# Performance work log

Measured on AMD Instinct MI355X. Metric: run time of the kernel, lower is better.

## Reference

```python
import jax, jax.numpy as jnp
import numpy as np

# --- config (matches init_kwargs) ---
D_MODEL = 512
N_HEADS = 8
DIM_HEAD = D_MODEL // N_HEADS  # 64
BUCKET_SIZE = 64
N_HASHES = 4
B = 4
N = 4096
SELF_ATTN_VALUE = -5e4  # TOKEN_SELF_ATTN_VALUE in reformer_pytorch


def setup_inputs() -> dict:
    key = jax.random.key(0)
    ks = jax.random.split(key, 8)
    n_buckets = N // BUCKET_SIZE
    dh = N_HEADS * DIM_HEAD
    return {
        "queries": jax.random.normal(ks[0], (B, N, D_MODEL), jnp.float32),
        "keys": jax.random.normal(ks[1], (B, N, D_MODEL), jnp.float32),      # unused by module
        "values": jax.random.normal(ks[2], (B, N, D_MODEL), jnp.float32),    # unused by module
        "W_qk": jax.random.normal(ks[3], (D_MODEL, dh), jnp.float32) / np.float32(np.sqrt(D_MODEL)),
        "W_v": jax.random.normal(ks[4], (D_MODEL, dh), jnp.float32) / np.float32(np.sqrt(D_MODEL)),
        "W_out": jax.random.normal(ks[5], (dh, D_MODEL), jnp.float32) / np.float32(np.sqrt(dh)),
        "b_out": jnp.zeros((D_MODEL,), jnp.float32),
        # random LSH rotations: generated fresh (non-learnable) in torch; fixed here for determinism
        "rotations": jax.random.normal(ks[6], (DIM_HEAD, N_HASHES, n_buckets // 2), jnp.float32),
    }


def _look_one_back(x):
    # concat each chunk with the previous chunk along the within-chunk axis
    return jnp.concatenate([x, jnp.roll(x, 1, axis=1)], axis=2)


def lsh_attention(qk, v, rotations):
    # qk, v: (BH, T, dh) shared-QK LSH attention (reformer_pytorch LSHAttention)
    bh, T, dh = qk.shape
    n_buckets = T // BUCKET_SIZE
    total = N_HASHES * T

    # --- hash_vectors: random rotations + argmax over [R, -R] ---
    rotated = jnp.einsum('btf,fhi->bhti', qk, rotations)          # (bh, n_hashes, T, nb/2)
    rotated = jnp.concatenate([rotated, -rotated], axis=-1)       # (bh, n_hashes, T, nb)
    buckets = jnp.argmax(rotated, axis=-1)                        # (bh, n_hashes, T)
    offsets = (jnp.arange(N_HASHES) * n_buckets)[None, :, None]
    buckets = (buckets + offsets).reshape(bh, total)

    # --- stable sort by (bucket, position); keys are unique ---
    ticker = jnp.broadcast_to(jnp.arange(total)[None, :], (bh, total))
    buckets_and_t = T * buckets + (ticker % T)
    sticker = jnp.argsort(buckets_and_t, axis=-1)                 # (bh, total)
    undo_sort = jnp.argsort(sticker, axis=-1)
    st = sticker % T                                              # original positions, sorted

    sqk = jnp.take_along_axis(qk, st[:, :, None], axis=1)         # (bh, total, dh)
    sv = jnp.take_along_axis(v, st[:, :, None], axis=1)

    # --- chunk into bins; attend within chunk + one chunk back ---
    chunks = N_HASHES * n_buckets                                 # per-chunk len == BUCKET_SIZE
    bq_t = st.reshape(bh, chunks, -1)
    bqk = sqk.reshape(bh, chunks, -1, dh)
    bv = sv.reshape(bh, chunks, -1, dh)

    bq = bqk
    bk = bqk / jnp.maximum(jnp.linalg.norm(bqk, axis=-1, keepdims=True), 1e-12)  # F.normalize

    bk = _look_one_back(bk)       # (bh, chunks, 2*bs, dh)
    bv = _look_one_back(bv)
    bkv_t = _look_one_back(bq_t)  # (bh, chunks, 2*bs)

    dots = jnp.einsum('bcie,bcje->bcij', bq, bk) * (dh ** -0.5)   # (bh, chunks, bs, 2*bs)
    self_mask = bq_t[:, :, :, None] == bkv_t[:, :, None, :]
    dots = jnp.where(self_mask, SELF_ATTN_VALUE, dots)

    lse = jax.scipy.special.logsumexp(dots, axis=-1, keepdims=True)
    probs = jnp.exp(dots - lse)
    bo = jnp.einsum('bcij,bcje->bcie', probs, bv)                 # (bh, chunks, bs, dh)

    so = bo.reshape(bh, total, dh)
    slogits = lse.reshape(bh, total)
    o = jnp.take_along_axis(so, undo_sort[:, :, None], axis=1)
    logits = jnp.take_along_axis(slogits, undo_sort, axis=1)

    o = o.reshape(bh, N_HASHES, T, dh)
    logits = logits.reshape(bh, N_HASHES, T, 1)
    # combine hash rounds by softmax over per-round logsumexps
    w = jnp.exp(logits - jax.scipy.special.logsumexp(logits, axis=1, keepdims=True))
    return jnp.sum(o * w, axis=1)                                 # (bh, T, dh)


def reference(queries, keys, values, W_qk, W_v, W_out, b_out, rotations):
    Bsz, T, _ = queries.shape
    qk = queries @ W_qk                                           # (B, T, H*dh), no bias
    v = queries @ W_v

    def merge(x):
        return x.reshape(Bsz, T, N_HEADS, DIM_HEAD).transpose(0, 2, 1, 3).reshape(Bsz * N_HEADS, T, DIM_HEAD)

    out = lsh_attention(merge(qk), merge(v), rotations)           # (B*H, T, dh)
    out = out.reshape(Bsz, N_HEADS, T, DIM_HEAD).transpose(0, 2, 1, 3).reshape(Bsz, T, N_HEADS * DIM_HEAD)
    return out @ W_out + b_out                                    # to_out (with bias)
```

## Files before the change

### kernel.cpp

```cpp
#include <hip/hip_runtime.h>

typedef unsigned int uint32;
typedef _Float16 f16;
typedef _Float16 f16x8 __attribute__((ext_vector_type(8)));
typedef float f32x4 __attribute__((ext_vector_type(4)));
typedef unsigned short u16x8 __attribute__((ext_vector_type(8)));

#define B_SZ 4
#define T_SZ 4096
#define DMODEL 512
#define NHEAD 8
#define DH 64
#define NHASH 4
#define BH (B_SZ*NHEAD)
#define NBUCK 256
#define TOT (NHASH*T_SZ)
#define M_TOK (B_SZ*T_SZ)

#define KSTRIDE 72
#define PSTRIDE 136

#define AMB_TAU 1.5e-3f

__global__ __launch_bounds__(256) void kprep(
    const float* __restrict__ Wqk, const float* __restrict__ Wv,
    const float* __restrict__ Wout, f16* __restrict__ Wth, f16* __restrict__ Wtl,
    const float* __restrict__ rot, f16* __restrict__ rotTh, f16* __restrict__ rotTl,
    const float* __restrict__ qin, f16* __restrict__ Ah, f16* __restrict__ Al,
    int* __restrict__ amb_cnt)
{
  int bx = blockIdx.x;
  if (bx == 0 && threadIdx.x == 0) *amb_cnt = 0;
  if (bx < 3072){
    int gid = bx*256 + threadIdx.x;
    int n = gid >> 9, k = gid & 511;
    int sel = n >> 9, col = n & 511;
    const float* src = (sel==0)? Wqk : (sel==1)? Wv : Wout;
    float v = src[(size_t)k*512 + col];
    f16 h = (f16)v;
    Wth[gid] = h;
    Wtl[gid] = (f16)(v - (float)h);
  } else if (bx < 3104){
    int gid = (bx - 3072)*256 + threadIdx.x;
    int n = gid >> 6, dd = gid & 63;
    float v = rot[dd*128 + n];
    f16 h = (f16)v;
    rotTh[gid] = h;
    rotTl[gid] = (f16)(v - (float)h);
  } else {
    size_t gid = (size_t)(bx - 3104)*256 + threadIdx.x;
    const float4* src = (const float4*)(qin) + gid*2;
    float4 x0 = src[0], x1 = src[1];
    float v[8] = {x0.x,x0.y,x0.z,x0.w, x1.x,x1.y,x1.z,x1.w};
    f16x8 h, l;
    #pragma unroll
    for (int e=0;e<8;e++){ f16 hh=(f16)v[e]; h[e]=hh; l[e]=(f16)(v[e]-(float)hh); }
    ((f16x8*)Ah)[gid] = h;
    ((f16x8*)Al)[gid] = l;
  }
}

__global__ __launch_bounds__(256) void g_qkv(const f16* __restrict__ Ah,
    const f16* __restrict__ Al, const f16* __restrict__ Wth, const f16* __restrict__ Wtl,
    f16* __restrict__ qk16, f16* __restrict__ qkl, f16* __restrict__ v16)
{
  __shared__ f16 ah[128*KSTRIDE], al[128*KSTRIDE], bh[128*KSTRIDE], bl[128*KSTRIDE];
  int tid = threadIdx.x;
  int m0 = blockIdx.x*128, n0 = blockIdx.y*128;
  int w = tid >> 6, lane = tid & 63;
  int wm = w >> 1, wn = w & 1;
  int c_lane = lane & 15, quad = lane >> 4;

  f32x4 acc[4][4];
  #pragma unroll
  for (int mi=0;mi<4;mi++)
    #pragma unroll
    for (int ni=0;ni<4;ni++) acc[mi][ni] = (f32x4){0.f,0.f,0.f,0.f};

  int sr = tid >> 1, sc = (tid & 1) * 32;
  for (int kc=0; kc<8; kc++){
    int k0 = kc*64;
    {
      const f16x8* pah = (const f16x8*)(Ah + (size_t)(m0+sr)*512 + k0 + sc);
      const f16x8* pal = (const f16x8*)(Al + (size_t)(m0+sr)*512 + k0 + sc);
      const f16x8* pbh = (const f16x8*)(Wth + (size_t)(n0+sr)*512 + k0 + sc);
      const f16x8* pbl = (const f16x8*)(Wtl + (size_t)(n0+sr)*512 + k0 + sc);
      f16x8* dah = (f16x8*)&ah[sr*KSTRIDE + sc];
      f16x8* dal = (f16x8*)&al[sr*KSTRIDE + sc];
      f16x8* dbh = (f16x8*)&bh[sr*KSTRIDE + sc];
      f16x8* dbl = (f16x8*)&bl[sr*KSTRIDE + sc];
      #pragma unroll
      for (int i=0;i<4;i++){ dah[i]=pah[i]; dal[i]=pal[i]; dbh[i]=pbh[i]; dbl[i]=pbl[i]; }
    }
    __syncthreads();
    f16x8 fah[4][2], fal[4][2], fbh[4][2], fbl[4][2];
    #pragma unroll
    for (int i=0;i<4;i++)
      #pragma unroll
      for (int kb=0;kb<2;kb++){
        int ma = (wm*64 + i*16 + c_lane)*KSTRIDE + kb*32 + quad*8;
        int nb = (wn*64 + i*16 + c_lane)*KSTRIDE + kb*32 + quad*8;
        fah[i][kb] = *(const f16x8*)&ah[ma];
        fal[i][kb] = *(const f16x8*)&al[ma];
        fbh[i][kb] = *(const f16x8*)&bh[nb];
        fbl[i][kb] = *(const f16x8*)&bl[nb];
      }
    #pragma unroll
    for (int kb=0;kb<2;kb++)
      #pragma unroll
      for (int p=0;p<3;p++)
        #pragma unroll
        for (int mi=0;mi<4;mi++)
          #pragma unroll
          for (int ni=0;ni<4;ni++){
            f16x8 a = (p==2)? fal[mi][kb] : fah[mi][kb];
            f16x8 b = (p==1)? fbl[ni][kb] : fbh[ni][kb];
            acc[mi][ni] = __builtin_amdgcn_mfma_f32_16x16x32_f16(a, b, acc[mi][ni], 0,0,0);
          }
    __syncthreads();
  }

  #pragma unroll
  for (int mi=0;mi<4;mi++)
    #pragma unroll
    for (int ni=0;ni<4;ni++)
      #pragma unroll
      for (int r=0;r<4;r++){
        int n = n0 + wn*64 + ni*16 + c_lane;
        int tok = m0 + wm*64 + mi*16 + quad*4 + r;
        float val = acc[mi][ni][r];
        int b = tok >> 12, tp = tok & 4095;
        if (n < 512){
          int head = n >> 6, dd = n & 63;
          size_t idx = ((size_t)(b*NHEAD+head)*T_SZ + tp)*DH + dd;
          f16 hv = (f16)val;
          qk16[idx] = hv;
          qkl[idx]  = (f16)(val - (float)hv);
        } else {
          int j = n - 512, head = j >> 6, dd = j & 63;
          size_t idx = ((size_t)(b*NHEAD+head)*T_SZ + tp)*DH + dd;
          v16[idx] = (f16)val;
        }
      }
}

__global__ __launch_bounds__(256) void g_out(const float* __restrict__ lse,
    const f16* __restrict__ o_f16, const f16* __restrict__ Wth, const f16* __restrict__ Wtl,
    const float* __restrict__ bout, float* __restrict__ out)
{
  __shared__ f16 ah[128*KSTRIDE], al[128*KSTRIDE];
  int tid = threadIdx.x;
  int m0 = blockIdx.x*128, n0 = blockIdx.y*128;
  int w = tid >> 6, lane = tid & 63;
  int wm = w >> 1, wn = w & 1;
  int c_lane = lane & 15, quad = lane >> 4;
  const f16* Bh_base = Wth + (size_t)1024*512;
  const f16* Bl_base = Wtl + (size_t)1024*512;

  f32x4 acc[4][4];
  #pragma unroll
  for (int mi=0;mi<4;mi++)
    #pragma unroll
    for (int ni=0;ni<4;ni++) acc[mi][ni] = (f32x4){0.f,0.f,0.f,0.f};

  int sr = tid >> 1, sc = (tid & 1) * 32;
  int tok = m0 + sr;
  int tb = tok >> 12, tt = tok & 4095;

  for (int kc=0; kc<8; kc++){
    int k0 = kc*64;
    {
      size_t lbase = ((size_t)(tb*NHEAD + kc)*NHASH)*T_SZ + tt;
      float l0 = lse[lbase];
      float l1 = lse[lbase + T_SZ];
      float l2 = lse[lbase + 2*T_SZ];
      float l3 = lse[lbase + 3*T_SZ];
      float M = fmaxf(fmaxf(l0,l1), fmaxf(l2,l3));
      float e0 = __expf(l0-M), e1 = __expf(l1-M), e2 = __expf(l2-M), e3 = __expf(l3-M);
      float inv = 1.0f/(e0+e1+e2+e3);
      float w0=e0*inv, w1=e1*inv, w2=e2*inv, w3=e3*inv;
      const f16x8* r0 = (const f16x8*)(o_f16 + lbase*DH + sc);
      const f16x8* r1 = (const f16x8*)(o_f16 + (lbase + (size_t)T_SZ)*DH + sc);
      const f16x8* r2 = (const f16x8*)(o_f16 + (lbase + (size_t)2*T_SZ)*DH + sc);
      const f16x8* r3 = (const f16x8*)(o_f16 + (lbase + (size_t)3*T_SZ)*DH + sc);
      f16x8* dah = (f16x8*)&ah[sr*KSTRIDE + sc];
      f16x8* dal = (f16x8*)&al[sr*KSTRIDE + sc];
      #pragma unroll
      for (int i=0;i<4;i++){
        f16x8 a = r0[i], bb = r1[i], cc = r2[i], dd = r3[i];
        f16x8 ho, lo;
        #pragma unroll
        for (int e=0;e<8;e++){
          float res = w0*(float)a[e] + w1*(float)bb[e] + w2*(float)cc[e] + w3*(float)dd[e];
          f16 hh = (f16)res;
          ho[e] = hh; lo[e] = (f16)(res - (float)hh);
        }
        dah[i] = ho; dal[i] = lo;
      }
    }
    __syncthreads();
    f16x8 fah[4][2], fal[4][2], fbh[4][2], fbl[4][2];
    #pragma unroll
    for (int i=0;i<4;i++){
      int ma = (wm*64 + i*16 + c_lane)*KSTRIDE;
      const f16* brh = Bh_base + (size_t)(n0 + wn*64 + i*16 + c_lane)*512 + k0;
      const f16* brl = Bl_base + (size_t)(n0 + wn*64 + i*16 + c_lane)*512 + k0;
      #pragma unroll
      for (int kb=0;kb<2;kb++){
        fah[i][kb] = *(const f16x8*)&ah[ma + kb*32 + quad*8];
        fal[i][kb] = *(const f16x8*)&al[ma + kb*32 + quad*8];
        fbh[i][kb] = *(const f16x8*)&brh[kb*32 + quad*8];
        fbl[i][kb] = *(const f16x8*)&brl[kb*32 + quad*8];
      }
    }
    #pragma unroll
    for (int kb=0;kb<2;kb++)
      #pragma unroll
      for (int p=0;p<3;p++)
        #pragma unroll
        for (int mi=0;mi<4;mi++)
          #pragma unroll
          for (int ni=0;ni<4;ni++){
            f16x8 a = (p==2)? fal[mi][kb] : fah[mi][kb];
            f16x8 b = (p==1)? fbl[ni][kb] : fbh[ni][kb];
            acc[mi][ni] = __builtin_amdgcn_mfma_f32_16x16x32_f16(a, b, acc[mi][ni], 0,0,0);
          }
    __syncthreads();
  }

  #pragma unroll
  for (int mi=0;mi<4;mi++)
    #pragma unroll
    for (int ni=0;ni<4;ni++){
      int n = n0 + wn*64 + ni*16 + c_lane;
      float bn = bout[n];
      #pragma unroll
      for (int r=0;r<4;r++){
        int tk2 = m0 + wm*64 + mi*16 + quad*4 + r;
        out[(size_t)tk2*512 + n] = acc[mi][ni][r] + bn;
      }
    }
}

__global__ __launch_bounds__(256, 4) void k2_mfma(const f16* __restrict__ qkh,
    const f16* __restrict__ qkl, const f16* __restrict__ rotTh, const f16* __restrict__ rotTl,
    unsigned short* __restrict__ bucket,
    int* __restrict__ amb_list, int* __restrict__ amb_cnt)
{
  int tid = threadIdx.x;
  int w = tid >> 6, lane = tid & 63;
  int c_lane = lane & 15, quad = lane >> 4;
  int tok0 = (blockIdx.x*4 + w)*16;
  size_t rowb = (size_t)(tok0 + c_lane)*64;

  f16x8 tbh[2], tbl[2];
  #pragma unroll
  for (int kb=0;kb<2;kb++){
    tbh[kb] = *(const f16x8*)&qkh[rowb + kb*32 + quad*8];
    tbl[kb] = *(const f16x8*)&qkl[rowb + kb*32 + quad*8];
  }

  f32x4 acc[8];
  #pragma unroll
  for (int mi=0;mi<8;mi++) acc[mi] = (f32x4){0.f,0.f,0.f,0.f};

  #pragma unroll
  for (int mi=0;mi<8;mi++){
    int aoff = (mi*16 + c_lane)*64;
    #pragma unroll
    for (int kb=0;kb<2;kb++){
      f16x8 arh = *(const f16x8*)&rotTh[aoff + kb*32 + quad*8];
      f16x8 arl = *(const f16x8*)&rotTl[aoff + kb*32 + quad*8];
      acc[mi] = __builtin_amdgcn_mfma_f32_16x16x32_f16(arh, tbh[kb], acc[mi], 0,0,0);
      acc[mi] = __builtin_amdgcn_mfma_f32_16x16x32_f16(arl, tbh[kb], acc[mi], 0,0,0);
      acc[mi] = __builtin_amdgcn_mfma_f32_16x16x32_f16(arh, tbl[kb], acc[mi], 0,0,0);
    }
  }

  int tokg = tok0 + c_lane;
  int bhh = tokg >> 12, t = tokg & 4095;

  #pragma unroll
  for (int h=0; h<4; h++){
    float m1 = -1e30f, m2 = -1e30f, ssq = 0.f; int b1 = 0;
    #pragma unroll
    for (int u=0; u<8; u++){
      float v = acc[2*h + (u>>2)][u&3];
      int bidd = (u>>2)*16 + quad*4 + (u&3);
      ssq += v*v;
      if (v > m1){ m2=m1; m1=v; b1=bidd; } else if (v > m2) m2=v;
      float nv = -v;
      if (nv > m1){ m2=m1; m1=nv; b1=bidd+32; } else if (nv > m2) m2=nv;
    }
    #pragma unroll
    for (int d2=16; d2<64; d2<<=1){
      float om1 = __shfl_xor(m1, d2);
      float om2 = __shfl_xor(m2, d2);
      int   ob1 = __shfl_xor(b1, d2);
      ssq += __shfl_xor(ssq, d2);
      if (om1 > m1){ m2 = fmaxf(m1, om2); m1 = om1; b1 = ob1; }
      else          { m2 = fmaxf(m2, om1); }
    }
    if (quad == 0){
      float rms = sqrtf(ssq * (1.0f/32.0f));
      if (m1 - m2 < AMB_TAU * rms){
        int idx = atomicAdd(amb_cnt, 1);
        amb_list[idx] = (bhh<<14) | (h<<12) | t;
      } else {
        bucket[((bhh*NHASH + h)<<12) + t] = (unsigned short)(b1 + (h<<6));
      }
    }
  }
}

__global__ __launch_bounds__(256) void k2_fix(const float* __restrict__ qin,
    const float* __restrict__ Wqk, const float* __restrict__ rot,
    const int* __restrict__ amb_list, const int* __restrict__ amb_cnt,
    unsigned short* __restrict__ bucket)
{
  __shared__ __align__(16) float qs[512];
  __shared__ double part[4][64];
  __shared__ double qk64[64];
  __shared__ double accs[32];
  int n = *amb_cnt;
  int tid = threadIdx.x;
  int j = tid & 63, chunk = tid >> 6;
  for (int it = blockIdx.x; it < n; it += gridDim.x){
    int gid = amb_list[it];
    int t = gid & (T_SZ-1);
    int h = (gid >> 12) & 3;
    int bh = gid >> 14;
    int b = bh >> 3, head = bh & 7;
    if (tid < 128)
      *(float4*)&qs[tid*4] = ((const float4*)(qin + ((size_t)b*T_SZ + t)*DMODEL))[tid];
    __syncthreads();
    const float* wcol = Wqk + head*64 + j;
    int d0 = chunk*128;
    double s = 0.0;
    #pragma unroll 16
    for (int d=0; d<128; d++)
      s += (double)qs[d0+d] * (double)wcol[(size_t)(d0+d)*512];
    part[chunk][j] = s;
    __syncthreads();
    if (tid < 64)
      qk64[tid] = ((part[0][tid] + part[1][tid]) + part[2][tid]) + part[3][tid];
    __syncthreads();
    if (tid < 32){
      double a = 0.0;
      #pragma unroll 16
      for (int f=0; f<64; f++)
        a += qk64[f] * (double)rot[f*(NHASH*32) + h*32 + tid];
      accs[tid] = a;
    }
    __syncthreads();
    if (tid == 0){
      double best = accs[0]; int bk = 0;
      for (int k=1;k<64;k++){
        double vv = (k<32)? accs[k] : -accs[k-32];
        if (vv > best){ best = vv; bk = k; }
      }
      bucket[((bh*NHASH + h)<<12) + t] = (unsigned short)(bk + (h<<6));
    }
    __syncthreads();
  }
}

__global__ __launch_bounds__(256) void k3_scan(const unsigned short* __restrict__ bucket,
    int* __restrict__ starts){
  __shared__ int s[256];
  int bh = blockIdx.x, tid = threadIdx.x;
  s[tid] = 0;
  __syncthreads();
  const u16x8* b8 = (const u16x8*)(bucket + ((size_t)bh*NHASH << 12));
  for (int i = tid; i < 2048; i += 256){
    u16x8 x = b8[i];
    #pragma unroll
    for (int e=0;e<8;e++) atomicAdd(&s[x[e]], 1);
  }
  __syncthreads();
  int v = s[tid];
  __syncthreads();
  for (int off=1; off<256; off<<=1){
    int a = (tid >= off) ? s[tid-off] : 0;
    __syncthreads();
    s[tid] += a;
    __syncthreads();
  }
  starts[bh*256 + tid] = s[tid] - v;
}

__global__ __launch_bounds__(64) void k3b_scatter(const unsigned short* __restrict__ bucket,
    const int* __restrict__ starts, int* __restrict__ st)
{
  int blk = blockIdx.x;
  int bh = blk >> 8; int g = blk & 255; int h = g >> 6;
  int lane = threadIdx.x;
  const unsigned short* brow = bucket + ((bh*NHASH + h)<<12);
  int base = starts[bh*NBUCK + g];
  for (int step=0; step<64; step++){
    int t = step*64 + lane;
    bool pred = (brow[t] == (unsigned short)g);
    unsigned long long mask = __ballot(pred);
    if (pred){
      int off = __popcll(mask & ((1ull<<lane) - 1ull));
      st[bh*TOT + base + off] = t;
    }
    base += __popcll(mask);
  }
}

__global__ __launch_bounds__(256, 4) void k4_attn(const f16* __restrict__ qk16,
    const f16* __restrict__ v16, const int* __restrict__ st,
    float* __restrict__ lse_out, f16* __restrict__ o_out)
{
  __shared__ __align__(16) char smem[36864];
  f16*   k_lds   = (f16*)smem;
  f16*   p_lds   = (f16*)smem;
  f16*   vT      = (f16*)(smem + 18432);
  float* invnorm = (float*)(smem + 35840);
  int*   kv_t    = (int*)(smem + 36352);

  int bid = blockIdx.x;
  int swz = (bid & 7) * 1024 + (bid >> 3);
  int bh = swz >> 8; int c = swz & 255;
  int h = c >> 6; int cp = (c + 255) & 255;
  int tid = threadIdx.x;
  int w = tid >> 6, lane = tid & 63;
  int c_lane = lane & 15, quad = lane >> 4;
  const int* strow = st + bh*TOT;

  if (tid < 128){
    int row = tid;
    int slot = (row < 64) ? (c*64 + row) : (cp*64 + row - 64);
    int t = strow[slot];
    kv_t[row] = t;
    const f16x8* kr = (const f16x8*)(qk16 + ((size_t)bh*T_SZ + t)*DH);
    const f16x8* vr = (const f16x8*)(v16  + ((size_t)bh*T_SZ + t)*DH);
    f16x8 kv[8], vv[8];
    float ss = 0.f;
    #pragma unroll
    for (int i=0;i<8;i++){
      f16x8 x = kr[i]; kv[i] = x;
      vv[i] = vr[i];
      #pragma unroll
      for (int e=0;e<8;e++){ float f = (float)x[e]; ss += f*f; }
    }
    invnorm[row] = 1.0f / fmaxf(sqrtf(ss), 1e-12f);
    f16x8* kd = (f16x8*)&k_lds[row*KSTRIDE];
    #pragma unroll
    for (int i=0;i<8;i++) kd[i] = kv[i];
    #pragma unroll
    for (int i=0;i<8;i++){
      #pragma unroll
      for (int e=0;e<8;e++) vT[(i*8+e)*PSTRIDE + row] = vv[i][e];
    }
  }
  __syncthreads();

  int mi = w;
  f16x8 aq[2];
  #pragma unroll
  for (int kb=0;kb<2;kb++)
    aq[kb] = *(const f16x8*)&k_lds[(mi*16 + c_lane)*KSTRIDE + kb*32 + quad*8];

  f32x4 accS[8];
  #pragma unroll
  for (int ni=0;ni<8;ni++) accS[ni] = (f32x4){0.f,0.f,0.f,0.f};

  #pragma unroll
  for (int ni=0;ni<8;ni++){
    int rowb = ni*16 + c_lane;
    f16 sc = (f16)invnorm[rowb];
    f16x8 b0 = *(const f16x8*)&k_lds[rowb*KSTRIDE + 0*32 + quad*8];
    f16x8 b1 = *(const f16x8*)&k_lds[rowb*KSTRIDE + 1*32 + quad*8];
    b0 *= sc; b1 *= sc;
    accS[ni] = __builtin_amdgcn_mfma_f32_16x16x32_f16(aq[0], b0, accS[ni], 0,0,0);
    accS[ni] = __builtin_amdgcn_mfma_f32_16x16x32_f16(aq[1], b1, accS[ni], 0,0,0);
  }

  int tq[4];
  #pragma unroll
  for (int r=0;r<4;r++) tq[r] = kv_t[mi*16 + quad*4 + r];
  int tk[8];
  #pragma unroll
  for (int ni=0;ni<8;ni++) tk[ni] = kv_t[ni*16 + c_lane];

  float mrow[4], lrow[4];
  #pragma unroll
  for (int r=0;r<4;r++){
    float mx = -1e30f;
    #pragma unroll
    for (int ni=0;ni<8;ni++){
      float s = accS[ni][r] * 0.125f;
      if (tk[ni] == tq[r]) s = -50000.0f;
      accS[ni][r] = s;
      mx = fmaxf(mx, s);
    }
    mx = fmaxf(mx, __shfl_xor(mx, 1));
    mx = fmaxf(mx, __shfl_xor(mx, 2));
    mx = fmaxf(mx, __shfl_xor(mx, 4));
    mx = fmaxf(mx, __shfl_xor(mx, 8));
    mrow[r] = mx;
    float ls = 0.f;
    #pragma unroll
    for (int ni=0;ni<8;ni++){
      float e = __expf(accS[ni][r] - mx);
      accS[ni][r] = e;
      ls += e;
    }
    ls += __shfl_xor(ls, 1);
    ls += __shfl_xor(ls, 2);
    ls += __shfl_xor(ls, 4);
    ls += __shfl_xor(ls, 8);
    lrow[r] = ls;
  }

  __syncthreads();

  #pragma unroll
  for (int ni=0;ni<8;ni++)
    #pragma unroll
    for (int r=0;r<4;r++)
      p_lds[(mi*16 + quad*4 + r)*PSTRIDE + ni*16 + c_lane] = (f16)accS[ni][r];

  f16x8 pa[4];
  #pragma unroll
  for (int kb=0;kb<4;kb++)
    pa[kb] = *(const f16x8*)&p_lds[(mi*16 + c_lane)*PSTRIDE + kb*32 + quad*8];

  size_t rowbase = (size_t)(bh*NHASH + h)*T_SZ;
  #pragma unroll
  for (int ni2=0;ni2<4;ni2++){
    f16x8 bv[4];
    #pragma unroll
    for (int kb=0;kb<4;kb++)
      bv[kb] = *(const f16x8*)&vT[(ni2*16 + c_lane)*PSTRIDE + kb*32 + quad*8];
    f32x4 accO = (f32x4){0.f,0.f,0.f,0.f};
    #pragma unroll
    for (int kb=0;kb<4;kb++)
      accO = __builtin_amdgcn_mfma_f32_16x16x32_f16(pa[kb], bv[kb], accO, 0,0,0);
    #pragma unroll
    for (int r=0;r<4;r++){
      float invl = 1.0f / lrow[r];
      f16* orow = o_out + (rowbase + tq[r])*DH;
      orow[ni2*16 + c_lane] = (f16)(accO[r] * invl);
    }
  }
  #pragma unroll
  for (int r=0;r<4;r++){
    if (c_lane == 0)
      lse_out[rowbase + tq[r]] = mrow[r] + logf(lrow[r]);
  }
}

extern "C" void kernel_launch(void* const* d_in, const int* in_sizes, int n_in,
                              void* d_out, int out_size, void* d_ws, size_t ws_size,
                              hipStream_t stream) {
  const float* queries = (const float*)d_in[0];
  const float* Wqk     = (const float*)d_in[3];
  const float* Wv      = (const float*)d_in[4];
  const float* Wout    = (const float*)d_in[5];
  const float* bout    = (const float*)d_in[6];
  const float* rot     = (const float*)d_in[7];
  float* out = (float*)d_out;

  const size_t SZ_F16  = (size_t)BH*T_SZ*DH*2;
  const size_t SZ_WT   = (size_t)1536*512*2;
  const size_t SZ_ROT  = (size_t)128*64*2;
  const size_t SZ_O    = (size_t)BH*NHASH*T_SZ*DH*2;
  const size_t OFS_X      = 0;
  const size_t OFS_AH     = OFS_X    + 2*SZ_F16;
  const size_t OFS_AL     = OFS_AH   + SZ_F16;
  const size_t OFS_QK16   = OFS_AL   + SZ_F16;
  const size_t OFS_V16    = OFS_QK16 + SZ_F16;
  const size_t OFS_WTH    = OFS_V16  + SZ_F16;
  const size_t OFS_WTL    = OFS_WTH  + SZ_WT;
  const size_t OFS_ROTH   = OFS_WTL  + SZ_WT;
  const size_t OFS_ROTL   = OFS_ROTH + SZ_ROT;
  const size_t OFS_O      = OFS_ROTL + SZ_ROT;
  const size_t OFS_BUCKET = OFS_O    + SZ_O;
  const size_t OFS_HIST   = OFS_BUCKET + (size_t)BH*NHASH*T_SZ*2;
  const size_t OFS_STARTS = OFS_HIST   + (size_t)BH*NBUCK*4;
  const size_t OFS_ST     = OFS_STARTS + (size_t)BH*NBUCK*4;
  const size_t OFS_LSE    = OFS_ST     + (size_t)BH*TOT*4;
  const size_t OFS_AMB    = OFS_LSE    + (size_t)BH*NHASH*T_SZ*4;
  const size_t OFS_CNT    = OFS_AMB    + (size_t)BH*NHASH*T_SZ*4;
  const size_t WS_NEEDED  = OFS_CNT    + 256;
  if (ws_size < WS_NEEDED) return;

  char* ws = (char*)d_ws;
  f16*      qkl    = (f16*)(ws + OFS_X);
  f16*      Ah     = (f16*)(ws + OFS_AH);
  f16*      Al     = (f16*)(ws + OFS_AL);
  f16*      qk16   = (f16*)(ws + OFS_QK16);
  f16*      v16    = (f16*)(ws + OFS_V16);
  f16*      Wth    = (f16*)(ws + OFS_WTH);
  f16*      Wtl    = (f16*)(ws + OFS_WTL);
  f16*      rotTh  = (f16*)(ws + OFS_ROTH);
  f16*      rotTl  = (f16*)(ws + OFS_ROTL);
  f16*      o_f16  = (f16*)(ws + OFS_O);
  unsigned short* bucket = (unsigned short*)(ws + OFS_BUCKET);
  int*      starts = (int*)(ws + OFS_STARTS);
  int*      st     = (int*)(ws + OFS_ST);
  float*    lse    = (float*)(ws + OFS_LSE);
  int*      amb    = (int*)(ws + OFS_AMB);
  int*      cnt    = (int*)(ws + OFS_CNT);

  kprep     <<<7200, 256, 0, stream>>>(Wqk, Wv, Wout, Wth, Wtl, rot, rotTh, rotTl,
                                       queries, Ah, Al, cnt);
  g_qkv     <<<dim3(M_TOK/128, 8), 256, 0, stream>>>(Ah, Al, Wth, Wtl, qk16, qkl, v16);
  k2_mfma   <<<(BH*T_SZ)/64, 256, 0, stream>>>(qk16, qkl, rotTh, rotTl, bucket, amb, cnt);
  k2_fix    <<<2048, 256, 0, stream>>>(queries, Wqk, rot, amb, cnt, bucket);
  k3_scan   <<<BH, 256, 0, stream>>>(bucket, starts);
  k3b_scatter<<<BH*NBUCK, 64, 0, stream>>>(bucket, starts, st);
  k4_attn   <<<BH*256, 256, 0, stream>>>(qk16, v16, st, lse, o_f16);
  g_out     <<<dim3(M_TOK/128, 4), 256, 0, stream>>>(lse, o_f16, Wth, Wtl, bout, out);
}
```

Measured before the change: 456.5 us.

## Stage W_out tiles in shared memory and prefetch next A chunk in g_out

The output-projection GEMM kernel now loads the W_out hi/lo tiles cooperatively into shared memory, replacing per-wave direct global loads of B fragments. It also issues the next k-chunk's lse and o_f16 global loads into registers right after the barrier, so they overlap the MFMA work of the current chunk. This is meant to cut redundant global traffic for B and hide global-load latency for A. In exchange it doubles shared memory per block and raises register pressure from the prefetch buffers, which may lower occupancy.

Measured after the change: 433.9 us. 4.9% less time.

```diff
diff --git a/kernel.cpp b/kernel.cpp
--- a/kernel.cpp
+++ b/kernel.cpp
@@ -148,7 +148,7 @@
     const f16* __restrict__ o_f16, const f16* __restrict__ Wth, const f16* __restrict__ Wtl,
     const float* __restrict__ bout, float* __restrict__ out)
 {
-  __shared__ f16 ah[128*KSTRIDE], al[128*KSTRIDE];
+  __shared__ f16 ah[128*KSTRIDE], al[128*KSTRIDE], bh[128*KSTRIDE], bl[128*KSTRIDE];
   int tid = threadIdx.x;
   int m0 = blockIdx.x*128, n0 = blockIdx.y*128;
   int w = tid >> 6, lane = tid & 63;
@@ -167,27 +167,41 @@
   int tok = m0 + sr;
   int tb = tok >> 12, tt = tok & 4095;
 
+  float pl0, pl1, pl2, pl3;
+  f16x8 pr0[4], pr1[4], pr2[4], pr3[4];
+
+  auto issueA = [&](int kc){
+    size_t lbase = ((size_t)(tb*NHEAD + kc)*NHASH)*T_SZ + tt;
+    pl0 = lse[lbase];
+    pl1 = lse[lbase + T_SZ];
+    pl2 = lse[lbase + 2*T_SZ];
+    pl3 = lse[lbase + 3*T_SZ];
+    const f16x8* r0 = (const f16x8*)(o_f16 + lbase*DH + sc);
+    const f16x8* r1 = (const f16x8*)(o_f16 + (lbase + (size_t)T_SZ)*DH + sc);
+    const f16x8* r2 = (const f16x8*)(o_f16 + (lbase + (size_t)2*T_SZ)*DH + sc);
+    const f16x8* r3 = (const f16x8*)(o_f16 + (lbase + (size_t)3*T_SZ)*DH + sc);
+    #pragma unroll
+    for (int i=0;i<4;i++){ pr0[i]=r0[i]; pr1[i]=r1[i]; pr2[i]=r2[i]; pr3[i]=r3[i]; }
+  };
+
+  issueA(0);
+
   for (int kc=0; kc<8; kc++){
     int k0 = kc*64;
     {
-      size_t lbase = ((size_t)(tb*NHEAD + kc)*NHASH)*T_SZ + tt;
-      float l0 = lse[lbase];
-      float l1 = lse[lbase + T_SZ];
-      float l2 = lse[lbase + 2*T_SZ];
-      float l3 = lse[lbase + 3*T_SZ];
-      float M = fmaxf(fmaxf(l0,l1), fmaxf(l2,l3));
-      float e0 = __expf(l0-M), e1 = __expf(l1-M), e2 = __expf(l2-M), e3 = __expf(l3-M);
+      float M = fmaxf(fmaxf(pl0,pl1), fmaxf(pl2,pl3));
+      float e0 = __expf(pl0-M), e1 = __expf(pl1-M), e2 = __expf(pl2-M), e3 = __expf(pl3-M);
       float inv = 1.0f/(e0+e1+e2+e3);
       float w0=e0*inv, w1=e1*inv, w2=e2*inv, w3=e3*inv;
-      const f16x8* r0 = (const f16x8*)(o_f16 + lbase*DH + sc);
-      const f16x8* r1 = (const f16x8*)(o_f16 + (lbase + (size_t)T_SZ)*DH + sc);
-      const f16x8* r2 = (const f16x8*)(o_f16 + (lbase + (size_t)2*T_SZ)*DH + sc);
-      const f16x8* r3 = (const f16x8*)(o_f16 + (lbase + (size_t)3*T_SZ)*DH + sc);
+      const f16x8* pbhp = (const f16x8*)(Bh_base + (size_t)(n0+sr)*512 + k0 + sc);
+      const f16x8* pblp = (const f16x8*)(Bl_base + (size_t)(n0+sr)*512 + k0 + sc);
       f16x8* dah = (f16x8*)&ah[sr*KSTRIDE + sc];
       f16x8* dal = (f16x8*)&al[sr*KSTRIDE + sc];
+      f16x8* dbh = (f16x8*)&bh[sr*KSTRIDE + sc];
+      f16x8* dbl = (f16x8*)&bl[sr*KSTRIDE + sc];
       #pragma unroll
       for (int i=0;i<4;i++){
-        f16x8 a = r0[i], bb = r1[i], cc = r2[i], dd = r3[i];
+        f16x8 a = pr0[i], bb = pr1[i], cc = pr2[i], dd = pr3[i];
         f16x8 ho, lo;
         #pragma unroll
         for (int e=0;e<8;e++){
@@ -196,23 +210,23 @@
           ho[e] = hh; lo[e] = (f16)(res - (float)hh);
         }
         dah[i] = ho; dal[i] = lo;
+        dbh[i] = pbhp[i]; dbl[i] = pblp[i];
       }
     }
     __syncthreads();
+    if (kc < 7) issueA(kc+1);
     f16x8 fah[4][2], fal[4][2], fbh[4][2], fbl[4][2];
     #pragma unroll
-    for (int i=0;i<4;i++){
-      int ma = (wm*64 + i*16 + c_lane)*KSTRIDE;
-      const f16* brh = Bh_base + (size_t)(n0 + wn*64 + i*16 + c_lane)*512 + k0;
-      const f16* brl = Bl_base + (size_t)(n0 + wn*64 + i*16 + c_lane)*512 + k0;
+    for (int i=0;i<4;i++)
       #pragma unroll
       for (int kb=0;kb<2;kb++){
-        fah[i][kb] = *(const f16x8*)&ah[ma + kb*32 + quad*8];
-        fal[i][kb] = *(const f16x8*)&al[ma + kb*32 + quad*8];
-        fbh[i][kb] = *(const f16x8*)&brh[kb*32 + quad*8];
-        fbl[i][kb] = *(const f16x8*)&brl[kb*32 + quad*8];
+        int ma = (wm*64 + i*16 + c_lane)*KSTRIDE + kb*32 + quad*8;
+        int nb = (wn*64 + i*16 + c_lane)*KSTRIDE + kb*32 + quad*8;
+        fah[i][kb] = *(const f16x8*)&ah[ma];
+        fal[i][kb] = *(const f16x8*)&al[ma];
+        fbh[i][kb] = *(const f16x8*)&bh[nb];
+        fbl[i][kb] = *(const f16x8*)&bl[nb];
       }
-    }
     #pragma unroll
     for (int kb=0;kb<2;kb++)
       #pragma unroll
```
